# Optimization experiments

Measured on AMD Instinct MI355X. Metric: run time of the kernel, lower is better.

## Reference

```python
import jax, jax.numpy as jnp
import numpy as np

EPS = 1e-5
SCALE = 12.0            # scale_factor passed to krahenbuhl2013.CRF
SXY_G = 3.0 / SCALE     # spatial Gaussian stddev
SXY_B = 80.0 / SCALE    # bilateral spatial stddev
SRGB = 13.0             # bilateral color stddev
COMPAT_G = 3.0          # Potts weight, Gaussian term
COMPAT_B = 10.0         # Potts weight, bilateral term
N_ITERS = 10            # mean-field iterations


def _softmax_clamped(score):
    # my_softmax: clamp(softmax, eps, 1) then renormalize over channel dim
    p = jnp.clip(jax.nn.softmax(score, axis=1), EPS, 1.0)
    return p / jnp.sum(p, axis=1, keepdims=True)


def _crf(images, probs):
    # images: (n,3,H,W), probs: (n,C,h,w). Dense-CRF mean-field refinement
    # (exact Gaussian kernels in place of permutohedral approximation).
    n, C, h, w = probs.shape
    N = h * w
    # nd.zoom(order=1): bilinear resize image to prob resolution, NHWC
    ims = jnp.transpose(images, (0, 2, 3, 1))
    ims = jax.image.resize(ims, (n, h, w, ims.shape[-1]), method='linear')
    colors = ims.reshape(n, N, -1)  # (n,N,3)
    # pixel grid positions
    yy, xx = jnp.meshgrid(jnp.arange(h, dtype=jnp.float32),
                          jnp.arange(w, dtype=jnp.float32), indexing='ij')
    pos = jnp.stack([xx.ravel(), yy.ravel()], axis=-1)      # (N,2)
    d2 = jnp.sum((pos[:, None] - pos[None]) ** 2, axis=-1)  # (N,N)
    not_self = 1.0 - jnp.eye(N, dtype=probs.dtype)          # exclude j==i (paper: sum over j!=i)
    Kg = jnp.exp(-d2 / (2.0 * SXY_G ** 2)) * not_self       # (N,N), shared over batch
    # bilateral color distance via gram trick: |Ii-Ij|^2 = |Ii|^2+|Ij|^2-2 Ii.Ij
    csq = jnp.sum(colors ** 2, axis=-1)                     # (n,N)
    cd2 = csq[:, :, None] + csq[:, None, :] - 2.0 * jnp.einsum('nic,njc->nij', colors, colors)
    cd2 = jnp.maximum(cd2, 0.0)
    Kb = jnp.exp(-d2[None] / (2.0 * SXY_B ** 2) - cd2 / (2.0 * SRGB ** 2)) * not_self  # (n,N,N)
    # symmetric kernel normalization (pydensecrf NORMALIZE_SYMMETRIC)
    sg = jnp.sum(Kg, axis=-1)
    Kg = Kg / jnp.sqrt(sg[:, None] * sg[None, :])
    sb = jnp.sum(Kb, axis=-1)
    Kb = Kb / jnp.sqrt(sb[:, :, None] * sb[:, None, :])
    logu = jnp.log(probs).reshape(n, C, N)  # = -unary energy
    Q0 = probs.reshape(n, C, N)

    def step(Q, _):
        mg = jnp.einsum('ij,ncj->nci', Kg, Q)   # spatial message
        mb = jnp.einsum('nij,ncj->nci', Kb, Q)  # bilateral message
        Q = jax.nn.softmax(logu + COMPAT_G * mg + COMPAT_B * mb, axis=1)
        return Q, None

    Q, _ = jax.lax.scan(step, Q0, None, length=N_ITERS)
    Q = Q.reshape(n, C, h, w)
    # crf_prob[crf_prob < eps] = eps; renormalize
    Q = jnp.maximum(Q, EPS)
    return Q / jnp.sum(Q, axis=1, keepdims=True)


def setup_inputs() -> dict:
    key = jax.random.key(0)
    k1, k2 = jax.random.split(key)
    images = jax.random.uniform(k1, (16, 3, 321, 321), dtype=jnp.float32) * 255.0
    predict = jax.random.normal(k2, (16, 21, 41, 41), dtype=jnp.float32)
    return {"images": images, "predict": predict}


def reference(images, predict):
    probs = _softmax_clamped(predict)
    # CRF result comes from numpy in the original -> detached from autograd
    probs_smooth = jax.lax.stop_gradient(_crf(images, probs))
    ratio = jnp.clip(probs_smooth / probs, 0.05, 20.0)
    loss = jnp.mean(jnp.sum(probs_smooth * jnp.log(ratio), axis=1))
    return loss
```

## Files before the change

kernel.cpp:

```cpp
#include <hip/hip_runtime.h>
#include <math.h>

namespace {

typedef unsigned short ushort_t;
typedef unsigned int uint_t;
typedef unsigned char uchar_t;
typedef __attribute__((ext_vector_type(4))) float f32x4;

constexpr int NBATCH = 16;
constexpr int NCH    = 21;
constexpr int HH     = 41;
constexpr int NP     = HH * HH;
constexpr int IW     = 321;
constexpr int QS     = 32;
constexpr float EPSV = 1e-5f;

constexpr int NROWS  = 1696;
constexpr int KPAD   = 1792;
constexpr int ITL    = 27;
constexpr int NPIX   = NBATCH * NP;
constexpr int LOSS_BLOCKS = (NPIX + 255) / 256;
constexpr int RSB_TILES = (NP + 63) / 64;

constexpr int QB_BATCH = 56 * 2 * 512;
constexpr int QB_BUF   = NBATCH * QB_BATCH;
constexpr int RXN = NBATCH * 3 * IW * HH;

constexpr float CS_COLOR = 0.06533245f;
constexpr float CS_XY    = 0.12739827f;
constexpr float KGC      = 711.111111f;
constexpr float L2E8     = 11.5415603f;
constexpr float GATE     = 0.138f;

constexpr size_t OFF_W    = 0;
constexpr size_t OFF_RX   = 13184;
constexpr size_t OFF_COL  = 644928;
constexpr size_t OFF_P    = 752512;
constexpr size_t OFF_LOGU = 1613184;
constexpr size_t OFF_QF   = 2473856;
constexpr size_t OFF_RSG  = 3334528;
constexpr size_t OFF_XY   = 3336256;
constexpr size_t OFF_PART = 3339712;
constexpr size_t OFF_QB   = 3339968;
constexpr size_t OFF_M    = 3798720;

constexpr size_t QB_ZERO_DWORDS = 458752;

#define GLOAD_LDS16(g, l)                                                              \
  __builtin_amdgcn_global_load_lds((const __attribute__((address_space(1))) uint_t*)(g), \
                                   (__attribute__((address_space(3))) uint_t*)(l), 16, 0, 0)

__device__ __forceinline__ float wave_sum(float v) {
  #pragma unroll
  for (int off = 32; off > 0; off >>= 1) v += __shfl_down(v, off, 64);
  return v;
}

__device__ __forceinline__ uchar_t f32_to_fp8(float f) {
  return (uchar_t)(__builtin_amdgcn_cvt_pk_fp8_f32(f, f, 0, false) & 0xff);
}

__global__ void k_zero(uint_t* __restrict__ p) {
  size_t t = (size_t)blockIdx.x * blockDim.x + threadIdx.x;
  if (t < QB_ZERO_DWORDS) p[t] = 0u;
}

__global__ void k_weights(float* __restrict__ W) {
  int o = threadIdx.x;
  if (o >= HH) return;
  const float inv = (float)IW / (float)HH;
  float s = (o + 0.5f) * inv - 0.5f;
  float tot = 0.f;
  for (int i = 0; i < IW; ++i) {
    float x = fabsf(s - (float)i) / inv;
    tot += fmaxf(0.f, 1.f - x);
  }
  float r = 1.f / tot;
  for (int i = 0; i < IW; ++i) {
    float x = fabsf(s - (float)i) / inv;
    W[o * IW + i] = fmaxf(0.f, 1.f - x) * r;
  }
}

__global__ void k_xy(float2* __restrict__ XY) {
  int j = blockIdx.x * blockDim.x + threadIdx.x;
  if (j >= NP) return;
  XY[j] = make_float2((float)(j % HH) * CS_XY, (float)(j / HH) * CS_XY);
}

__global__ void k_resize_x(const float* __restrict__ img, const float* __restrict__ W,
                           float* __restrict__ RX) {
  int t = blockIdx.x * blockDim.x + threadIdx.x;
  if (t >= RXN) return;
  int xo = t % HH;
  int rest = t / HH;
  int y = rest % IW;
  int nc = rest / IW;
  const float inv = (float)IW / (float)HH;
  float sx = (xo + 0.5f) * inv - 0.5f;
  int xlo = max(0, (int)ceilf(sx - inv)), xhi = min(IW - 1, (int)floorf(sx + inv));
  const float* base = img + ((size_t)nc * IW + y) * IW;
  const float* wr = W + xo * IW;
  float a = 0.f;
  for (int ix = xlo; ix <= xhi; ++ix) a += wr[ix] * base[ix];
  RX[t] = a;
}

__global__ void k_resize_y(const float* __restrict__ RX, const float* __restrict__ W,
                           float* __restrict__ colors) {
  int t = blockIdx.x * blockDim.x + threadIdx.x;
  if (t >= NPIX) return;
  int nb = t / NP, p = t % NP;
  int yo = p / HH, xo = p % HH;
  const float inv = (float)IW / (float)HH;
  float sy = (yo + 0.5f) * inv - 0.5f;
  int ylo = max(0, (int)ceilf(sy - inv)), yhi = min(IW - 1, (int)floorf(sy + inv));
  const float* wr = W + yo * IW;
  float a0 = 0.f, a1 = 0.f, a2 = 0.f;
  const float* b0 = RX + (size_t)(nb * 3 + 0) * IW * HH + xo;
  const float* b1 = RX + (size_t)(nb * 3 + 1) * IW * HH + xo;
  const float* b2 = RX + (size_t)(nb * 3 + 2) * IW * HH + xo;
  for (int iy = ylo; iy <= yhi; ++iy) {
    float wy = wr[iy];
    a0 += wy * b0[(size_t)iy * HH];
    a1 += wy * b1[(size_t)iy * HH];
    a2 += wy * b2[(size_t)iy * HH];
  }
  float* c = colors + (size_t)t * 4;
  c[0] = a0 * CS_COLOR; c[1] = a1 * CS_COLOR; c[2] = a2 * CS_COLOR; c[3] = 0.f;
}

__global__ void k_probs(const float* __restrict__ pred, float* __restrict__ P,
                        float* __restrict__ LOGU, uchar_t* __restrict__ QB) {
  int t = blockIdx.x * blockDim.x + threadIdx.x;
  if (t >= NPIX) return;
  int nb = t / NP, i = t % NP;
  const float* src = pred + (size_t)nb * NCH * NP + i;
  float v[NCH];
  float m = -1e30f;
  #pragma unroll
  for (int c = 0; c < NCH; ++c) { v[c] = src[(size_t)c * NP]; m = fmaxf(m, v[c]); }
  float s = 0.f;
  #pragma unroll
  for (int c = 0; c < NCH; ++c) { v[c] = expf(v[c] - m); s += v[c]; }
  float r = 1.f / s;
  float s2 = 0.f;
  #pragma unroll
  for (int c = 0; c < NCH; ++c) { v[c] = fminf(fmaxf(v[c] * r, EPSV), 1.0f); s2 += v[c]; }
  float r2 = 1.f / s2;
  float* dp = P + (size_t)t * QS;
  float* dl = LOGU + (size_t)t * QS;
  int kb = i >> 5, kr = i & 31, q2 = kr >> 3, j = kr & 7;
  size_t sb = (size_t)nb * QB_BATCH + (size_t)kb * 1024 + j;
  #pragma unroll
  for (int c = 0; c < NCH; ++c) {
    float p = v[c] * r2;
    dp[c] = p; dl[c] = logf(p);
    int ct = c >> 4;
    QB[sb + (size_t)ct * 512 + (q2 * 16 + (c & 15)) * 8] = f32_to_fp8(p);
  }
}

__global__ void k_rsg(float* __restrict__ rsg) {
  int i = blockIdx.x;
  int lane = threadIdx.x;
  int xi = i % HH, yi = i / HH;
  float s = 0.f;
  for (int j = lane; j < NP; j += 64) {
    if (j == i) continue;
    int xj = j % HH, yj = j / HH;
    float dx = (float)(xi - xj), dy = (float)(yi - yj);
    s += __builtin_amdgcn_exp2f(-L2E8 * (dx * dx + dy * dy));
  }
  s = wave_sum(s);
  if (lane == 0) rsg[i] = 1.f / sqrtf(s);
}

__global__ __launch_bounds__(512) void k_rsb(float4* __restrict__ COL,
                                             const float2* __restrict__ XY) {
  __shared__ float S8[NP * 8];
  __shared__ float Red2[8 * 64];
  const int nb = blockIdx.x / RSB_TILES;
  const int i0 = (blockIdx.x % RSB_TILES) * 64;
  const int tid = (int)threadIdx.x;
  const int lane = tid & 63, wv = tid >> 6;

  const float4* colb = COL + (size_t)nb * NP;
  for (int j = tid; j < NP; j += 512) {
    float4 c = colb[j];
    float2 xy = XY[j];
    *(float4*)&S8[j * 8]     = make_float4(c.x, c.y, c.z, 0.f);
    *(float4*)&S8[j * 8 + 4] = make_float4(xy.x, xy.y, 0.f, 0.f);
  }
  __syncthreads();

  const int i = i0 + lane;
  const int im = min(i, NP - 1);
  const float ci0 = S8[im * 8], ci1 = S8[im * 8 + 1], ci2 = S8[im * 8 + 2];
  const float xi = S8[im * 8 + 4], yi = S8[im * 8 + 5];

  float s = 0.f;
  for (int j = wv; j < NP; j += 8) {
    float4 a = *(const float4*)&S8[j * 8];
    float4 b = *(const float4*)&S8[j * 8 + 4];
    float dx = xi - b.x, dy = yi - b.y;
    float acc = dx * dx;
    acc = fmaf(dy, dy, acc);
    float e0 = ci0 - a.x, e1 = ci1 - a.y, e2 = ci2 - a.z;
    acc = fmaf(e0, e0, acc);
    acc = fmaf(e1, e1, acc);
    acc = fmaf(e2, e2, acc);
    s += __builtin_amdgcn_exp2f(-acc);
  }
  Red2[wv * 64 + lane] = s;
  __syncthreads();
  if (wv == 0 && i < NP) {
    float t = -1.0f;
    #pragma unroll
    for (int w = 0; w < 8; ++w) t += Red2[w * 64 + lane];
    ((float*)(COL + (size_t)nb * NP + i))[3] = 1.f / sqrtf(t);
  }
}

__global__ __launch_bounds__(256) void k_buildM(const float4* __restrict__ COL,
                                                const float* __restrict__ rsg,
                                                uchar_t* __restrict__ M) {
  int row = blockIdx.x;
  int nb = row / NP, i = row % NP;
  float4 ci = COL[row];
  float xi = (float)(i % HH) * CS_XY, yi = (float)(i / HH) * CS_XY;
  float sb = 10.f * ci.w;
  float sg = 3.f * rsg[i];
  const float4* colb = COL + (size_t)nb * NP;
  uint_t* Mrow = (uint_t*)(M + ((size_t)nb * NROWS + i) * KPAD);

  const float XW = 40.5f * CS_XY;
  const float X41 = 41.0f * CS_XY;
  int j0 = 4 * (int)threadIdx.x;
  float x = (float)(j0 % HH) * CS_XY;
  float y = (float)(j0 / HH) * CS_XY;

  for (int p = (int)threadIdx.x; p < 424; p += 256) {
    int jj = 4 * p;
    float xx = x, yy = y;
    float v[4];
    #pragma unroll
    for (int e = 0; e < 4; ++e) {
      int je = jj + e;
      int jc = min(je, NP - 1);
      float4 cj = colb[jc];
      float dx = xi - xx, dy = yi - yy;
      float axy = fmaf(dy, dy, dx * dx);
      float e0 = ci.x - cj.x, e1 = ci.y - cj.y, e2 = ci.z - cj.z;
      float acc = axy;
      acc = fmaf(e0, e0, acc);
      acc = fmaf(e1, e1, acc);
      acc = fmaf(e2, e2, acc);
      float val = __builtin_amdgcn_exp2f(-acc) * (sb * cj.w);
      if (axy < GATE) val = fmaf(__builtin_amdgcn_exp2f(-KGC * axy), sg * rsg[jc], val);
      v[e] = (je < NP && je != i) ? val : 0.f;
      xx += CS_XY;
      if (xx > XW) { xx = 0.f; yy += CS_XY; }
    }
    uint_t wrd = __builtin_amdgcn_cvt_pk_fp8_f32(v[0], v[1], 0, false);
    wrd = __builtin_amdgcn_cvt_pk_fp8_f32(v[2], v[3], (int)wrd, true);
    Mrow[p] = wrd;

    x += 40.f * CS_XY; y += 24.f * CS_XY;
    if (x > XW) { x -= X41; y += CS_XY; }
  }
}

__global__ __launch_bounds__(256) void k_iter(const uchar_t* __restrict__ M,
                                              const uchar_t* __restrict__ QBin,
                                              uchar_t* __restrict__ QBout,
                                              const float* __restrict__ LOGU,
                                              float* __restrict__ QF) {
  __shared__ uchar_t Abuf[64 * 256];
  __shared__ uchar_t Bbuf[8 * 1024];
  const int nb = blockIdx.x & 15;
  const int t0 = (blockIdx.x >> 4) * 64;
  const int tid = (int)threadIdx.x;
  const int lane = tid & 63;
  const int w = tid >> 6;
  const int mrow = lane & 15, quad = lane >> 4;

  f32x4 acc0 = {0.f, 0.f, 0.f, 0.f};
  f32x4 acc1 = {0.f, 0.f, 0.f, 0.f};

  const size_t Mrow0 = (size_t)(nb * NROWS + t0);
  const uchar_t* Qb = QBin + (size_t)nb * QB_BATCH;

  for (int kc = 0; kc < 7; ++kc) {
    #pragma unroll
    for (int t4 = 0; t4 < 4; ++t4) {
      int t = w * 4 + t4;
      int r = t * 4 + (lane >> 4);
      int ug = (lane & 15) ^ (r & 7);
      const uchar_t* g = M + (Mrow0 + r) * KPAD + kc * 256 + ug * 16;
      GLOAD_LDS16(g, Abuf + t * 1024);
    }
    #pragma unroll
    for (int t2 = 0; t2 < 2; ++t2) {
      int t = w * 2 + t2;
      const uchar_t* g = Qb + (size_t)kc * 8192 + t * 1024 + lane * 16;
      GLOAD_LDS16(g, Bbuf + t * 1024);
    }
    __syncthreads();
    #pragma unroll
    for (int c = 0; c < 8; ++c) {
      long a = *(const long*)(Abuf + (w * 16 + mrow) * 256 +
                              (((c * 2 + (quad >> 1)) ^ (mrow & 7)) * 16) + (quad & 1) * 8);
      long b0 = *(const long*)(Bbuf + c * 1024 + lane * 8);
      long b1 = *(const long*)(Bbuf + c * 1024 + 512 + lane * 8);
      acc0 = __builtin_amdgcn_mfma_f32_16x16x32_fp8_fp8(a, b0, acc0, 0, 0, 0);
      acc1 = __builtin_amdgcn_mfma_f32_16x16x32_fp8_fp8(a, b1, acc1, 0, 0, 0);
    }
    __syncthreads();
  }

  const bool c1ok = (mrow + 16) < NCH;
  #pragma unroll
  for (int reg = 0; reg < 4; ++reg) {
    int r = t0 + w * 16 + quad * 4 + reg;
    int rg = nb * NP + min(r, NP - 1);
    float tv0 = LOGU[(size_t)rg * QS + mrow] + acc0[reg];
    float tv1 = c1ok ? (LOGU[(size_t)rg * QS + 16 + mrow] + acc1[reg]) : -1e30f;
    float mx = fmaxf(tv0, tv1);
    mx = fmaxf(mx, __shfl_xor(mx, 1));
    mx = fmaxf(mx, __shfl_xor(mx, 2));
    mx = fmaxf(mx, __shfl_xor(mx, 4));
    mx = fmaxf(mx, __shfl_xor(mx, 8));
    float e0 = __expf(tv0 - mx);
    float e1 = c1ok ? __expf(tv1 - mx) : 0.f;
    float sm = e0 + e1;
    sm += __shfl_xor(sm, 1);
    sm += __shfl_xor(sm, 2);
    sm += __shfl_xor(sm, 4);
    sm += __shfl_xor(sm, 8);
    float rinv = 1.f / sm;
    if (r < NP) {
      int kb = r >> 5, kr = r & 31, q2 = kr >> 3, j = kr & 7;
      size_t sbo = (size_t)nb * QB_BATCH + (size_t)kb * 1024 + (q2 * 16 + mrow) * 8 + j;
      float q0 = e0 * rinv;
      QF[(size_t)(nb * NP + r) * QS + mrow] = q0;
      QBout[sbo] = f32_to_fp8(q0);
      if (c1ok) {
        float q1 = e1 * rinv;
        QF[(size_t)(nb * NP + r) * QS + 16 + mrow] = q1;
        QBout[sbo + 512] = f32_to_fp8(q1);
      }
    }
  }
}

__global__ void k_loss(const float* __restrict__ Qf, const float* __restrict__ P,
                       float* __restrict__ part) {
  int t = blockIdx.x * blockDim.x + threadIdx.x;
  float s = 0.f;
  if (t < NPIX) {
    const float* q = Qf + (size_t)t * QS;
    const float* p = P + (size_t)t * QS;
    float qv[NCH];
    float qsum = 0.f;
    #pragma unroll
    for (int c = 0; c < NCH; ++c) { qv[c] = fmaxf(q[c], EPSV); qsum += qv[c]; }
    float r = 1.f / qsum;
    #pragma unroll
    for (int c = 0; c < NCH; ++c) {
      float qs = qv[c] * r;
      float ratio = fminf(fmaxf(qs / p[c], 0.05f), 20.0f);
      s += qs * logf(ratio);
    }
  }
  __shared__ float red[256];
  red[threadIdx.x] = s;
  __syncthreads();
  for (int st = 128; st > 0; st >>= 1) {
    if ((int)threadIdx.x < st) red[threadIdx.x] += red[threadIdx.x + st];
    __syncthreads();
  }
  if (threadIdx.x == 0) part[blockIdx.x] = red[0];
}

__global__ void k_final(const float* __restrict__ part, float* __restrict__ out) {
  float s = 0.f;
  for (int k = threadIdx.x; k < LOSS_BLOCKS; k += 64) s += part[k];
  s = wave_sum(s);
  if (threadIdx.x == 0) out[0] = s / (float)NPIX;
}

}

extern "C" void kernel_launch(void* const* d_in, const int* in_sizes, int n_in,
                              void* d_out, int out_size, void* d_ws, size_t ws_size,
                              hipStream_t stream) {
  const float* images  = (const float*)d_in[0];
  const float* predict = (const float*)d_in[1];
  float* out = (float*)d_out;
  float* ws = (float*)d_ws;

  float*  W    = ws + OFF_W;
  float*  RX   = ws + OFF_RX;
  float4* COL  = (float4*)(ws + OFF_COL);
  float*  P    = ws + OFF_P;
  float*  LOGU = ws + OFF_LOGU;
  float*  QF   = ws + OFF_QF;
  float*  RSG  = ws + OFF_RSG;
  float2* XY   = (float2*)(ws + OFF_XY);
  float*  PART = ws + OFF_PART;
  uchar_t* QB_A = (uchar_t*)(ws + OFF_QB);
  uchar_t* QB_B = QB_A + (size_t)QB_BUF;
  uchar_t* M    = (uchar_t*)(ws + OFF_M);

  hipLaunchKernelGGL(k_zero, dim3((unsigned)((QB_ZERO_DWORDS + 255) / 256)), dim3(256), 0,
                     stream, (uint_t*)QB_A);
  hipLaunchKernelGGL(k_weights, dim3(1), dim3(64), 0, stream, W);
  hipLaunchKernelGGL(k_xy, dim3((NP + 255) / 256), dim3(256), 0, stream, XY);
  hipLaunchKernelGGL(k_resize_x, dim3((RXN + 255) / 256), dim3(256), 0, stream, images, W, RX);
  hipLaunchKernelGGL(k_resize_y, dim3(LOSS_BLOCKS), dim3(256), 0, stream, RX, W, (float*)COL);
  hipLaunchKernelGGL(k_probs, dim3(LOSS_BLOCKS), dim3(256), 0, stream, predict, P, LOGU, QB_A);
  hipLaunchKernelGGL(k_rsg, dim3(NP), dim3(64), 0, stream, RSG);
  hipLaunchKernelGGL(k_rsb, dim3(NBATCH * RSB_TILES), dim3(512), 0, stream, COL, XY);
  hipLaunchKernelGGL(k_buildM, dim3(NPIX), dim3(256), 0, stream, COL, RSG, M);

  const uchar_t* qbin = QB_A;
  uchar_t* qbout = QB_B;
  for (int it = 0; it < 10; ++it) {
    hipLaunchKernelGGL(k_iter, dim3(NBATCH * ITL), dim3(256), 0, stream,
                       M, qbin, qbout, LOGU, QF);
    const uchar_t* t = qbout; qbout = (uchar_t*)qbin; qbin = t;
  }
  hipLaunchKernelGGL(k_loss, dim3(LOSS_BLOCKS), dim3(256), 0, stream, QF, P, PART);
  hipLaunchKernelGGL(k_final, dim3(1), dim3(64), 0, stream, PART, out);
}
```

Before: 332.2 us.

## Tile bilateral matrix build over row blocks and simplify iteration GEMM to direct loads

k_buildM now computes eight rows per block, reusing each loaded column/position across those rows. The per-pixel normaliser is folded into the exponent as a log term, replacing a multiply. The Gaussian spatial term is added only in a separate 5x5 neighbourhood pass instead of a gated branch in the inner loop. k_iter drops LDS staging and syncthreads in favour of one-wave blocks of 16 rows that load fp8 A/B fragments straight from global memory. The aim is lower build cost and less sync overhead per iteration, at the risk of poorer global load coalescing and less reuse of the Q operand in the GEMM.

```diff
diff --git a/kernel.cpp b/kernel.cpp
--- a/kernel.cpp
+++ b/kernel.cpp
@@ -18,20 +18,22 @@
 
 constexpr int NROWS  = 1696;
 constexpr int KPAD   = 1792;
-constexpr int ITL    = 27;
+constexpr int NKB    = 56;
+constexpr int ITL16  = 106;
 constexpr int NPIX   = NBATCH * NP;
 constexpr int LOSS_BLOCKS = (NPIX + 255) / 256;
 constexpr int RSB_TILES = (NP + 63) / 64;
-
-constexpr int QB_BATCH = 56 * 2 * 512;
+constexpr int BMROWS = 8;
+constexpr int BMTILES = (NP + BMROWS - 1) / BMROWS;
+
+constexpr int QB_BATCH = NKB * 2 * 512;
 constexpr int QB_BUF   = NBATCH * QB_BATCH;
 constexpr int RXN = NBATCH * 3 * IW * HH;
 
 constexpr float CS_COLOR = 0.06533245f;
 constexpr float CS_XY    = 0.12739827f;
-constexpr float KGC      = 711.111111f;
 constexpr float L2E8     = 11.5415603f;
-constexpr float GATE     = 0.138f;
+constexpr float HLOG2_10 = 1.6609640474f;
 
 constexpr size_t OFF_W    = 0;
 constexpr size_t OFF_RX   = 13184;
@@ -46,10 +48,6 @@
 constexpr size_t OFF_M    = 3798720;
 
 constexpr size_t QB_ZERO_DWORDS = 458752;
-
-#define GLOAD_LDS16(g, l)                                                              \
-  __builtin_amdgcn_global_load_lds((const __attribute__((address_space(1))) uint_t*)(g), \
-                                   (__attribute__((address_space(3))) uint_t*)(l), 16, 0, 0)
 
 __device__ __forceinline__ float wave_sum(float v) {
   #pragma unroll
@@ -219,111 +217,121 @@
     float t = -1.0f;
     #pragma unroll
     for (int w = 0; w < 8; ++w) t += Red2[w * 64 + lane];
-    ((float*)(COL + (size_t)nb * NP + i))[3] = 1.f / sqrtf(t);
+    ((float*)(COL + (size_t)nb * NP + i))[3] = HLOG2_10 - 0.5f * __builtin_amdgcn_logf(t);
   }
 }
 
 __global__ __launch_bounds__(256) void k_buildM(const float4* __restrict__ COL,
+                                                const float2* __restrict__ XY,
                                                 const float* __restrict__ rsg,
                                                 uchar_t* __restrict__ M) {
-  int row = blockIdx.x;
-  int nb = row / NP, i = row % NP;
-  float4 ci = COL[row];
-  float xi = (float)(i % HH) * CS_XY, yi = (float)(i / HH) * CS_XY;
-  float sb = 10.f * ci.w;
-  float sg = 3.f * rsg[i];
+  const int nb = blockIdx.x / BMTILES;
+  const int i0 = (blockIdx.x % BMTILES) * BMROWS;
+  const int tid = (int)threadIdx.x;
+  const int nr = min(BMROWS, NP - i0);
+
+  float cx[BMROWS], cy[BMROWS], cz[BMROWS], wi[BMROWS], xi[BMROWS], yi[BMROWS];
+  #pragma unroll
+  for (int r = 0; r < BMROWS; ++r) {
+    int i = min(i0 + r, NP - 1);
+    float4 c = COL[(size_t)nb * NP + i];
+    float2 xy = XY[i];
+    cx[r] = c.x; cy[r] = c.y; cz[r] = c.z; wi[r] = c.w; xi[r] = xy.x; yi[r] = xy.y;
+  }
   const float4* colb = COL + (size_t)nb * NP;
-  uint_t* Mrow = (uint_t*)(M + ((size_t)nb * NROWS + i) * KPAD);
-
-  const float XW = 40.5f * CS_XY;
-  const float X41 = 41.0f * CS_XY;
-  int j0 = 4 * (int)threadIdx.x;
-  float x = (float)(j0 % HH) * CS_XY;
-  float y = (float)(j0 / HH) * CS_XY;
-
-  for (int p = (int)threadIdx.x; p < 424; p += 256) {
-    int jj = 4 * p;
-    float xx = x, yy = y;
-    float v[4];
+  uchar_t* Mb = M + (size_t)(nb * NROWS + i0) * KPAD;
+
+  for (int p = tid; p < 424; p += 256) {
+    int j0 = 4 * p;
+    float4 cj[4]; float2 xyj[4];
     #pragma unroll
     for (int e = 0; e < 4; ++e) {
-      int je = jj + e;
-      int jc = min(je, NP - 1);
-      float4 cj = colb[jc];
-      float dx = xi - xx, dy = yi - yy;
-      float axy = fmaf(dy, dy, dx * dx);
-      float e0 = ci.x - cj.x, e1 = ci.y - cj.y, e2 = ci.z - cj.z;
-      float acc = axy;
-      acc = fmaf(e0, e0, acc);
-      acc = fmaf(e1, e1, acc);
-      acc = fmaf(e2, e2, acc);
-      float val = __builtin_amdgcn_exp2f(-acc) * (sb * cj.w);
-      if (axy < GATE) val = fmaf(__builtin_amdgcn_exp2f(-KGC * axy), sg * rsg[jc], val);
-      v[e] = (je < NP && je != i) ? val : 0.f;
-      xx += CS_XY;
-      if (xx > XW) { xx = 0.f; yy += CS_XY; }
+      int jc = min(j0 + e, NP - 1);
+      cj[e] = colb[jc];
+      xyj[e] = XY[jc];
     }
-    uint_t wrd = __builtin_amdgcn_cvt_pk_fp8_f32(v[0], v[1], 0, false);
-    wrd = __builtin_amdgcn_cvt_pk_fp8_f32(v[2], v[3], (int)wrd, true);
-    Mrow[p] = wrd;
-
-    x += 40.f * CS_XY; y += 24.f * CS_XY;
-    if (x > XW) { x -= X41; y += CS_XY; }
-  }
-}
-
-__global__ __launch_bounds__(256) void k_iter(const uchar_t* __restrict__ M,
-                                              const uchar_t* __restrict__ QBin,
-                                              uchar_t* __restrict__ QBout,
-                                              const float* __restrict__ LOGU,
-                                              float* __restrict__ QF) {
-  __shared__ uchar_t Abuf[64 * 256];
-  __shared__ uchar_t Bbuf[8 * 1024];
+    for (int r = 0; r < nr; ++r) {
+      float v[4];
+      #pragma unroll
+      for (int e = 0; e < 4; ++e) {
+        float dx = xi[r] - xyj[e].x, dy = yi[r] - xyj[e].y;
+        float acc = wi[r] + cj[e].w;
+        acc = fmaf(-dx, dx, acc);
+        acc = fmaf(-dy, dy, acc);
+        float e0 = cx[r] - cj[e].x, e1 = cy[r] - cj[e].y, e2 = cz[r] - cj[e].z;
+        acc = fmaf(-e0, e0, acc);
+        acc = fmaf(-e1, e1, acc);
+        acc = fmaf(-e2, e2, acc);
+        float val = __builtin_amdgcn_exp2f(acc);
+        int je = j0 + e;
+        v[e] = (je < NP && je != i0 + r) ? val : 0.f;
+      }
+      uint_t wrd = __builtin_amdgcn_cvt_pk_fp8_f32(v[0], v[1], 0, false);
+      wrd = __builtin_amdgcn_cvt_pk_fp8_f32(v[2], v[3], (int)wrd, true);
+      *(uint_t*)(Mb + (size_t)r * KPAD + 4 * p) = wrd;
+    }
+  }
+  if (tid < nr * 24) {
+    int r = tid / 24, d = tid % 24;
+    *(uint_t*)(Mb + (size_t)r * KPAD + 1696 + 4 * d) = 0u;
+  }
+  __syncthreads();
+  if (tid < nr * 25) {
+    int r = tid / 25, n = tid % 25;
+    int i = i0 + r;
+    int dxp = n % 5 - 2, dyp = n / 5 - 2;
+    int xpi = i % HH, ypi = i / HH;
+    int xj = xpi + dxp, yj = ypi + dyp;
+    if ((dxp | dyp) != 0 && xj >= 0 && xj < HH && yj >= 0 && yj < HH) {
+      int j = yj * HH + xj;
+      float d2 = (float)(dxp * dxp + dyp * dyp);
+      float kg = 3.f * rsg[i] * rsg[j] * __builtin_amdgcn_exp2f(-L2E8 * d2);
+      float4 c = colb[j];
+      float2 xy = XY[j];
+      float dx = xi[r] - xy.x, dy = yi[r] - xy.y;
+      float acc = wi[r] + c.w;
+      acc = fmaf(-dx, dx, acc);
+      acc = fmaf(-dy, dy, acc);
+      float e0 = cx[r] - c.x, e1 = cy[r] - c.y, e2 = cz[r] - c.z;
+      acc = fmaf(-e0, e0, acc);
+      acc = fmaf(-e1, e1, acc);
+      acc = fmaf(-e2, e2, acc);
+      float val = __builtin_amdgcn_exp2f(acc) + kg;
+      Mb[(size_t)r * KPAD + j] = f32_to_fp8(val);
+    }
+  }
+}
+
+__global__ __launch_bounds__(64) void k_iter(const uchar_t* __restrict__ M,
+                                             const uchar_t* __restrict__ QBin,
+                                             uchar_t* __restrict__ QBout,
+                                             const float* __restrict__ LOGU,
+                                             float* __restrict__ QF) {
   const int nb = blockIdx.x & 15;
-  const int t0 = (blockIdx.x >> 4) * 64;
-  const int tid = (int)threadIdx.x;
-  const int lane = tid & 63;
-  const int w = tid >> 6;
+  const int t0 = (blockIdx.x >> 4) * 16;
+  const int lane = (int)threadIdx.x;
   const int mrow = lane & 15, quad = lane >> 4;
 
   f32x4 acc0 = {0.f, 0.f, 0.f, 0.f};
   f32x4 acc1 = {0.f, 0.f, 0.f, 0.f};
 
-  const size_t Mrow0 = (size_t)(nb * NROWS + t0);
-  const uchar_t* Qb = QBin + (size_t)nb * QB_BATCH;
-
-  for (int kc = 0; kc < 7; ++kc) {
-    #pragma unroll
-    for (int t4 = 0; t4 < 4; ++t4) {
-      int t = w * 4 + t4;
-      int r = t * 4 + (lane >> 4);
-      int ug = (lane & 15) ^ (r & 7);
-      const uchar_t* g = M + (Mrow0 + r) * KPAD + kc * 256 + ug * 16;
-      GLOAD_LDS16(g, Abuf + t * 1024);
-    }
-    #pragma unroll
-    for (int t2 = 0; t2 < 2; ++t2) {
-      int t = w * 2 + t2;
-      const uchar_t* g = Qb + (size_t)kc * 8192 + t * 1024 + lane * 16;
-      GLOAD_LDS16(g, Bbuf + t * 1024);
-    }
-    __syncthreads();
-    #pragma unroll
-    for (int c = 0; c < 8; ++c) {
-      long a = *(const long*)(Abuf + (w * 16 + mrow) * 256 +
-                              (((c * 2 + (quad >> 1)) ^ (mrow & 7)) * 16) + (quad & 1) * 8);
-      long b0 = *(const long*)(Bbuf + c * 1024 + lane * 8);
-      long b1 = *(const long*)(Bbuf + c * 1024 + 512 + lane * 8);
-      acc0 = __builtin_amdgcn_mfma_f32_16x16x32_fp8_fp8(a, b0, acc0, 0, 0, 0);
-      acc1 = __builtin_amdgcn_mfma_f32_16x16x32_fp8_fp8(a, b1, acc1, 0, 0, 0);
-    }
-    __syncthreads();
+  const uchar_t* Ap = M + (size_t)(nb * NROWS + t0 + mrow) * KPAD + quad * 8;
+  const uchar_t* Bp = QBin + (size_t)nb * QB_BATCH + lane * 8;
+
+  #pragma unroll 8
+  for (int kb = 0; kb < NKB; ++kb) {
+    long a  = *(const long*)(Ap);
+    long b0 = *(const long*)(Bp);
+    long b1 = *(const long*)(Bp + 512);
+    Ap += 32; Bp += 1024;
+    acc0 = __builtin_amdgcn_mfma_f32_16x16x32_fp8_fp8(a, b0, acc0, 0, 0, 0);
+    acc1 = __builtin_amdgcn_mfma_f32_16x16x32_fp8_fp8(a, b1, acc1, 0, 0, 0);
   }
 
   const bool c1ok = (mrow + 16) < NCH;
   #pragma unroll
   for (int reg = 0; reg < 4; ++reg) {
-    int r = t0 + w * 16 + quad * 4 + reg;
+    int r = t0 + quad * 4 + reg;
     int rg = nb * NP + min(r, NP - 1);
     float tv0 = LOGU[(size_t)rg * QS + mrow] + acc0[reg];
     float tv1 = c1ok ? (LOGU[(size_t)rg * QS + 16 + mrow] + acc1[reg]) : -1e30f;
@@ -423,12 +431,12 @@
   hipLaunchKernelGGL(k_probs, dim3(LOSS_BLOCKS), dim3(256), 0, stream, predict, P, LOGU, QB_A);
   hipLaunchKernelGGL(k_rsg, dim3(NP), dim3(64), 0, stream, RSG);
   hipLaunchKernelGGL(k_rsb, dim3(NBATCH * RSB_TILES), dim3(512), 0, stream, COL, XY);
-  hipLaunchKernelGGL(k_buildM, dim3(NPIX), dim3(256), 0, stream, COL, RSG, M);
+  hipLaunchKernelGGL(k_buildM, dim3(NBATCH * BMTILES), dim3(256), 0, stream, COL, XY, RSG, M);
 
   const uchar_t* qbin = QB_A;
   uchar_t* qbout = QB_B;
   for (int it = 0; it < 10; ++it) {
-    hipLaunchKernelGGL(k_iter, dim3(NBATCH * ITL), dim3(256), 0, stream,
+    hipLaunchKernelGGL(k_iter, dim3(ITL16 * NBATCH), dim3(64), 0, stream,
                        M, qbin, qbout, LOGU, QF);
     const uchar_t* t = qbout; qbout = (uchar_t*)qbin; qbin = t;
   }
```

Measured after the change: 433.3 us. 1.3x slower.
